# Kernel tuning notes

Measured on AMD Instinct MI355X. Metric: run time of the kernel, lower is better.

The kernel has to match this reference:

```python
import jax, jax.numpy as jnp
import numpy as np

B, T, I, H, O = 64, 512, 512, 512, 512

def setup_inputs() -> dict:
    key = jax.random.key(0)
    ks = jax.random.split(key, 8)
    s = lambda k, shape, fan: jax.random.normal(k, shape, dtype=jnp.float32) / np.sqrt(fan)
    return {
        "embeddings": jax.random.normal(ks[0], (B, T, I), dtype=jnp.float32),
        "last_logits": jax.random.normal(ks[1], (B, O), dtype=jnp.float32),
        "W_in": s(ks[2], (H, I), I),
        "b_in": jnp.zeros((H,), jnp.float32),
        "W_y": s(ks[3], (H, O), O),
        "b_y": jnp.zeros((H,), jnp.float32),
        "W_out": s(ks[4], (O, H), H),
        "b_out": jnp.zeros((O,), jnp.float32),
    }

def reference(embeddings, last_logits, W_in, b_in, W_y, b_y, W_out, b_out):
    # Precompute input projection for all timesteps: [B,T,H] -> scan axis [T,B,H]
    xin = jnp.einsum("bti,hi->bth", embeddings, W_in) + b_in
    xin = jnp.swapaxes(xin, 0, 1)  # [T,B,H]

    def step(y_t, xin_t):
        # Jordan cell: h_t = tanh(W_in x_t + W_y y_{t-1} + biases); y_t = W_out h_t + b_out
        h_t = jnp.tanh(xin_t + y_t @ W_y.T + b_y)
        y_new = h_t @ W_out.T + b_out
        return y_new, (h_t, y_new)

    y_last, (h_seq, y_seq) = jax.lax.scan(step, last_logits, xin)
    h = jnp.swapaxes(h_seq, 0, 1)  # [B,T,H]
    y = jnp.swapaxes(y_seq, 0, 1)  # [B,T,O]
    return h, y, y_last
```

## Files before the change

### kernel.cpp

```cpp
#include <hip/hip_runtime.h>
#include <hip/hip_bf16.h>
#include <stdint.h>

typedef unsigned short u16;
typedef unsigned int u32;
typedef unsigned long long u64;
typedef __attribute__((ext_vector_type(8))) short short8;
typedef __attribute__((ext_vector_type(4))) float f32x4;
typedef __attribute__((ext_vector_type(2))) float f32x2;
typedef __attribute__((ext_vector_type(4))) unsigned short u16x4;

__device__ __forceinline__ float bf2f(u16 h) {
    union { u32 u; float f; } c; c.u = ((u32)h) << 16; return c.f;
}
__device__ __forceinline__ u16 f2bf(float f) {
    union { float f; u32 u; } c; c.f = f;
    u32 u = c.u;
    return (u16)((u + 0x7fffu + ((u >> 16) & 1u)) >> 16);
}

__device__ __forceinline__ float fast_tanh(float x) {
    float ax = __builtin_fabsf(x);
    float arg = ax * 2.8853900817779268f;
    float p;
    asm("v_exp_f32 %0, %1" : "=v"(p) : "v"(arg));
    float q = p + 1.f;
    float r;
    asm("v_rcp_f32 %0, %1" : "=v"(r) : "v"(q));
    float t = 1.f - 2.f * r;
    return __builtin_copysignf(t, x);
}

__global__ void k_init(u32* h_ex) {
    uint4 v;
    v.x = 0x00010000u; v.y = 0x00010000u; v.z = 0x00010000u; v.w = 0x00010000u;
    ((uint4*)h_ex)[blockIdx.x * 256 + threadIdx.x] = v;
}

__global__ void k_c(const float* __restrict__ Wy, const float* __restrict__ bout,
                    const float* __restrict__ bin, const float* __restrict__ by,
                    float* __restrict__ cvec, float* __restrict__ biasE) {
    int i = blockIdx.x * 64 + threadIdx.x;
    const float* wr = Wy + (size_t)i * 512;
    float s = 0.f;
    for (int k = 0; k < 512; ++k) s += wr[k] * bout[k];
    cvec[i] = s;
    biasE[i] = s + bin[i] + by[i];
}

__global__ __launch_bounds__(512) void k_z0(const float* __restrict__ ll,
                                            const float* __restrict__ Wy,
                                            const float* __restrict__ cvec,
                                            float* __restrict__ z0mc) {
    __shared__ float lls[512];
    int b = blockIdx.x, i = threadIdx.x;
    lls[i] = ll[b * 512 + i];
    __syncthreads();
    const float* wr = Wy + (size_t)i * 512;
    float s = 0.f;
    for (int k = 0; k < 512; ++k) s += wr[k] * lls[k];
    z0mc[(size_t)b * 512 + i] = s - cvec[i];
}

__global__ __launch_bounds__(256) void k_split(const float* __restrict__ in,
                                               u16* __restrict__ hi,
                                               u16* __restrict__ lo) {
    int i = blockIdx.x * 256 + threadIdx.x;
    float v = in[i];
    u16 h = f2bf(v);
    hi[i] = h;
    lo[i] = f2bf(v - bf2f(h));
}

__global__ __launch_bounds__(256) void k_tsplit(const float* __restrict__ in,
                                                u16* __restrict__ hi,
                                                u16* __restrict__ lo) {
    __shared__ float tile[32][33];
    int bx = blockIdx.x, by = blockIdx.y;
    int tx = threadIdx.x & 31, ty = threadIdx.x >> 5;
    for (int i = 0; i < 32; i += 8)
        tile[ty + i][tx] = in[(size_t)(by * 32 + ty + i) * 512 + bx * 32 + tx];
    __syncthreads();
    for (int i = 0; i < 32; i += 8) {
        float v = tile[tx][ty + i];
        size_t idx = (size_t)(bx * 32 + ty + i) * 512 + by * 32 + tx;
        u16 h = f2bf(v);
        hi[idx] = h;
        lo[idx] = f2bf(v - bf2f(h));
    }
}

__global__ __launch_bounds__(256) void gemm3(
    const void* __restrict__ Aptr, int a_fp32,
    const u16* __restrict__ Bhi, const u16* __restrict__ Blo,
    u16* __restrict__ out_hi, u16* __restrict__ out_lo,
    float* __restrict__ out_f,
    const float* __restrict__ bias, int mode) {
    __shared__ u16 AsHi[128 * 32];
    __shared__ u16 AsLo[128 * 32];
    __shared__ u16 BsHi[128 * 32];
    __shared__ u16 BsLo[128 * 32];
    const int tid = threadIdx.x;
    const int lane = tid & 63;
    const int w = tid >> 6;
    const int wm = w & 1, wn = w >> 1;
    const int quad = lane >> 4, l15 = lane & 15;
    const int tx = blockIdx.x, tn = blockIdx.y;

    f32x4 acc[4][4];
    f32x4 zero4 = {0.f, 0.f, 0.f, 0.f};
#pragma unroll
    for (int i = 0; i < 4; ++i)
#pragma unroll
        for (int j = 0; j < 4; ++j) acc[i][j] = zero4;

    const float* Af = (const float*)Aptr;
    const u16* Ab = (const u16*)Aptr;
    const int s0 = tid, s1 = tid + 256;

    for (int kk = 0; kk < 16; ++kk) {
        const uint4* BgH = (const uint4*)(Bhi + (size_t)tn * 128 * 512 + kk * 32);
        const uint4* BgL = (const uint4*)(Blo + (size_t)tn * 128 * 512 + kk * 32);
        uint4 bh0 = BgH[(s0 >> 2) * 64 + (s0 & 3)];
        uint4 bh1 = BgH[(s1 >> 2) * 64 + (s1 & 3)];
        uint4 bl0 = BgL[(s0 >> 2) * 64 + (s0 & 3)];
        uint4 bl1 = BgL[(s1 >> 2) * 64 + (s1 & 3)];
        f32x4 av[4];
        uint4 ab0, ab1;
        if (a_fp32) {
            const float* Agf = Af + (size_t)tx * 128 * 512 + kk * 32;
#pragma unroll
            for (int p = 0; p < 4; ++p) {
                int f = tid + p * 256;
                av[p] = *(const f32x4*)(Agf + (f >> 3) * 512 + (f & 7) * 4);
            }
        } else {
            const uint4* Ag = (const uint4*)(Ab + (size_t)tx * 128 * 512 + kk * 32);
            ab0 = Ag[(s0 >> 2) * 64 + (s0 & 3)];
            ab1 = Ag[(s1 >> 2) * 64 + (s1 & 3)];
        }
        __syncthreads();
        ((uint4*)BsHi)[s0] = bh0; ((uint4*)BsHi)[s1] = bh1;
        ((uint4*)BsLo)[s0] = bl0; ((uint4*)BsLo)[s1] = bl1;
        if (a_fp32) {
#pragma unroll
            for (int p = 0; p < 4; ++p) {
                int f = tid + p * 256;
                u16x4 hi4, lo4;
#pragma unroll
                for (int j = 0; j < 4; ++j) {
                    float v = av[p][j];
                    u16 hh = f2bf(v);
                    hi4[j] = hh;
                    lo4[j] = f2bf(v - bf2f(hh));
                }
                int off = (f >> 3) * 32 + (f & 7) * 4;
                *(u16x4*)(AsHi + off) = hi4;
                *(u16x4*)(AsLo + off) = lo4;
            }
        } else {
            ((uint4*)AsHi)[s0] = ab0;
            ((uint4*)AsHi)[s1] = ab1;
        }
        __syncthreads();

        short8 afh[4], afl[4], bfh[4], bfl[4];
#pragma unroll
        for (int mi = 0; mi < 4; ++mi) {
            afh[mi] = *(const short8*)(AsHi + (wm * 64 + mi * 16 + l15) * 32 + quad * 8);
            if (a_fp32)
                afl[mi] = *(const short8*)(AsLo + (wm * 64 + mi * 16 + l15) * 32 + quad * 8);
        }
#pragma unroll
        for (int ni = 0; ni < 4; ++ni) {
            bfh[ni] = *(const short8*)(BsHi + (wn * 64 + ni * 16 + l15) * 32 + quad * 8);
            bfl[ni] = *(const short8*)(BsLo + (wn * 64 + ni * 16 + l15) * 32 + quad * 8);
        }
#pragma unroll
        for (int mi = 0; mi < 4; ++mi)
#pragma unroll
            for (int ni = 0; ni < 4; ++ni) {
                acc[mi][ni] = __builtin_amdgcn_mfma_f32_16x16x32_bf16(
                    afh[mi], bfh[ni], acc[mi][ni], 0, 0, 0);
                acc[mi][ni] = __builtin_amdgcn_mfma_f32_16x16x32_bf16(
                    afh[mi], bfl[ni], acc[mi][ni], 0, 0, 0);
                if (a_fp32)
                    acc[mi][ni] = __builtin_amdgcn_mfma_f32_16x16x32_bf16(
                        afl[mi], bfh[ni], acc[mi][ni], 0, 0, 0);
            }
    }

#pragma unroll
    for (int mi = 0; mi < 4; ++mi) {
#pragma unroll
        for (int ni = 0; ni < 4; ++ni) {
            int col = tn * 128 + wn * 64 + ni * 16 + l15;
            float bv = (mode == 1) ? bias[col] : 0.f;
#pragma unroll
            for (int r = 0; r < 4; ++r) {
                int row = tx * 128 + wm * 64 + mi * 16 + quad * 4 + r;
                float v = acc[mi][ni][r] + bv;
                size_t idx = (size_t)row * 512 + col;
                if (mode == 0) {
                    u16 hi = f2bf(v);
                    out_hi[idx] = hi;
                    out_lo[idx] = f2bf(v - bf2f(hi));
                } else {
                    out_f[idx] = v;
                }
            }
        }
    }
}

__global__ __launch_bounds__(256, 1) void k_scan(
    const u16* __restrict__ Mhi, const u16* __restrict__ Mlo,
    float* e_io,
    const float* __restrict__ z0mc,
    u32* h_ex)
{
    __shared__ float zpart[2 * 4 * 4 * 64];

    const int tid = threadIdx.x;
    const int lane = tid & 63, w = tid >> 6;
    const int quad = lane >> 4, l15 = lane & 15;
    const int g = blockIdx.x & 3, s = blockIdx.x >> 2;

    short8 mf[2][4][2];
#pragma unroll
    for (int nt = 0; nt < 2; ++nt)
#pragma unroll
        for (int kap = 0; kap < 4; ++kap) {
            size_t off = ((size_t)(s * 32 + nt * 16 + l15)) * 512 +
                         (w * 128 + kap * 32 + quad * 8);
            mf[nt][kap][0] = *(const short8*)(Mhi + off);
            mf[nt][kap][1] = *(const short8*)(Mlo + off);
        }

    const int erow = tid >> 4;
    const int ec0 = (tid & 15) * 2;
    const int bb = g * 16 + erow;

    f32x2 ecur = *(const f32x2*)(e_io + ((size_t)bb * 512 + 0) * 512 + s * 32 + ec0);

#pragma unroll 1
    for (int t = 0; t < 512; ++t) {
        if (t > 0) {
            const u64* ex = (const u64*)(h_ex +
                (size_t)(((t - 1) & 1) * 4 + g) * 8192);
            const u64* p0 = ex + (size_t)(l15 * 512 + w * 128 + quad * 8) / 2;
            const u64 tagmask = (1ull << 16) | (1ull << 48);
            const u64 tagval = (((t - 1) >> 1) & 1) ? tagmask : 0ull;
            {
                const u64* pc = p0 + (size_t)quad * 16;
                for (;;) {
                    u64 c = __hip_atomic_load(pc, __ATOMIC_RELAXED,
                                              __HIP_MEMORY_SCOPE_AGENT);
                    if (__all(((c ^ tagval) & tagmask) == 0)) break;
                }
            }
            u64 d[4][4];
            for (;;) {
#pragma unroll
                for (int kap = 0; kap < 4; ++kap) {
                    const u64* p = p0 + kap * 16;
#pragma unroll
                    for (int j = 0; j < 4; ++j)
                        d[kap][j] = __hip_atomic_load(p + j, __ATOMIC_RELAXED,
                                                      __HIP_MEMORY_SCOPE_AGENT);
                }
                u64 bad = 0;
#pragma unroll
                for (int kap = 0; kap < 4; ++kap)
#pragma unroll
                    for (int j = 0; j < 4; ++j)
                        bad |= (d[kap][j] ^ tagval) & tagmask;
                if (__all(bad == 0)) break;
            }
            f32x4 accA[2], accB[2];
            f32x4 zero4 = {0.f, 0.f, 0.f, 0.f};
            accA[0] = zero4; accA[1] = zero4;
            accB[0] = zero4; accB[1] = zero4;
#pragma unroll
            for (int kap = 0; kap < 4; ++kap) {
                u32 qs[8] = {(u32)d[kap][0], (u32)(d[kap][0] >> 32),
                             (u32)d[kap][1], (u32)(d[kap][1] >> 32),
                             (u32)d[kap][2], (u32)(d[kap][2] >> 32),
                             (u32)d[kap][3], (u32)(d[kap][3] >> 32)};
                short8 ahi, alo;
#pragma unroll
                for (int j = 0; j < 8; ++j) {
                    ahi[j] = (short)(qs[j] & 0xffffu);
                    alo[j] = (short)(qs[j] >> 16);
                }
#pragma unroll
                for (int nt = 0; nt < 2; ++nt) {
                    f32x4* a = (kap < 2) ? &accA[nt] : &accB[nt];
                    *a = __builtin_amdgcn_mfma_f32_16x16x32_bf16(
                        ahi, mf[nt][kap][0], *a, 0, 0, 0);
                    *a = __builtin_amdgcn_mfma_f32_16x16x32_bf16(
                        alo, mf[nt][kap][0], *a, 0, 0, 0);
                    *a = __builtin_amdgcn_mfma_f32_16x16x32_bf16(
                        ahi, mf[nt][kap][1], *a, 0, 0, 0);
                }
            }
#pragma unroll
            for (int nt = 0; nt < 2; ++nt)
#pragma unroll
                for (int r = 0; r < 4; ++r)
                    zpart[((nt * 4 + w) * 4 + r) * 64 + lane] =
                        accA[nt][r] + accB[nt][r];
        }
        __syncthreads();

        {
            float hv[2];
#pragma unroll
            for (int cc = 0; cc < 2; ++cc) {
                int col = ec0 + cc;
                float z;
                if (t == 0) {
                    z = z0mc[(size_t)bb * 512 + s * 32 + col];
                } else {
                    int nt = col >> 4;
                    int lp = (erow >> 2) * 16 + (col & 15);
                    int rg = erow & 3;
                    z = zpart[((nt * 4 + 0) * 4 + rg) * 64 + lp] +
                        zpart[((nt * 4 + 1) * 4 + rg) * 64 + lp] +
                        zpart[((nt * 4 + 2) * 4 + rg) * 64 + lp] +
                        zpart[((nt * 4 + 3) * 4 + rg) * 64 + lp];
                }
                hv[cc] = fast_tanh(z + ecur[cc]);
            }
            u32 tag = (u32)((t >> 1) & 1);
            u32 pk[2];
#pragma unroll
            for (int cc = 0; cc < 2; ++cc) {
                u16 hi = f2bf(hv[cc]);
                u16 lo = f2bf(hv[cc] - bf2f(hi));
                lo = (u16)((lo & 0xFFFEu) | tag);
                pk[cc] = (((u32)lo) << 16) | (u32)hi;
            }
            u64 val = ((u64)pk[1] << 32) | pk[0];
            u64* dst = (u64*)(h_ex + (size_t)((t & 1) * 4 + g) * 8192 +
                              erow * 512 + s * 32 + ec0);
            __hip_atomic_store(dst, val, __ATOMIC_RELAXED,
                               __HIP_MEMORY_SCOPE_AGENT);
            size_t idx = ((size_t)bb * 512 + t) * 512 + s * 32 + ec0;
            f32x2 hw; hw[0] = hv[0]; hw[1] = hv[1];
            *(f32x2*)(e_io + idx) = hw;
            if (t < 511)
                ecur = *(const f32x2*)(e_io + idx + 512);
        }
        __asm__ volatile("" ::: "memory");
        __builtin_amdgcn_s_barrier();
        __asm__ volatile("" ::: "memory");
    }
}

__global__ __launch_bounds__(512) void k_ylast(const float* __restrict__ yreg,
                                               float* __restrict__ ylast) {
    int b = blockIdx.x, o = threadIdx.x;
    ylast[(size_t)b * 512 + o] = yreg[((size_t)b * 512 + 511) * 512 + o];
}

extern "C" void kernel_launch(void* const* d_in, const int* in_sizes, int n_in,
                              void* d_out, int out_size, void* d_ws, size_t ws_size,
                              hipStream_t stream) {
    const float* emb  = (const float*)d_in[0];
    const float* ll   = (const float*)d_in[1];
    const float* Win  = (const float*)d_in[2];
    const float* bin  = (const float*)d_in[3];
    const float* Wy   = (const float*)d_in[4];
    const float* by   = (const float*)d_in[5];
    const float* Wout = (const float*)d_in[6];
    const float* bout = (const float*)d_in[7];

    float* out = (float*)d_out;
    float* h_reg = out;
    float* y_reg = out + (size_t)16777216;
    float* ylast_reg = out + (size_t)33554432;

    char* ws = (char*)d_ws;
    size_t off = 0;
    u16* buf1 = (u16*)(ws + off); off += (size_t)512 * 512 * 2;
    u16* buf2 = (u16*)(ws + off); off += (size_t)512 * 512 * 2;
    u16* Mhi  = (u16*)(ws + off); off += (size_t)512 * 512 * 2;
    u16* Mlo  = (u16*)(ws + off); off += (size_t)512 * 512 * 2;
    float* z0mc  = (float*)(ws + off); off += (size_t)64 * 512 * 4;
    float* cvec  = (float*)(ws + off); off += 512 * 4;
    float* biasE = (float*)(ws + off); off += 512 * 4;
    u32* h_ex = (u32*)(ws + off); off += (size_t)2 * 4 * 8192 * 4;

    k_init<<<64, 256, 0, stream>>>(h_ex);
    k_c<<<8, 64, 0, stream>>>(Wy, bout, bin, by, cvec, biasE);
    k_z0<<<64, 512, 0, stream>>>(ll, Wy, cvec, z0mc);
    k_tsplit<<<dim3(16, 16), 256, 0, stream>>>(Wout, buf1, buf2);
    gemm3<<<dim3(4, 4), 256, 0, stream>>>(Wy, 1, buf1, buf2, Mhi, Mlo,
                                          nullptr, nullptr, 0);
    k_split<<<1024, 256, 0, stream>>>(Win, buf1, buf2);
    gemm3<<<dim3(256, 4), 256, 0, stream>>>(emb, 1, buf1, buf2, nullptr, nullptr,
                                            h_reg, biasE, 1);
    k_scan<<<64, 256, 0, stream>>>(Mhi, Mlo, h_reg, z0mc, h_ex);
    k_split<<<1024, 256, 0, stream>>>(Wout, buf1, buf2);
    gemm3<<<dim3(256, 4), 256, 0, stream>>>(h_reg, 1, buf1, buf2, nullptr, nullptr,
                                            y_reg, bout, 1);
    k_ylast<<<64, 512, 0, stream>>>(y_reg, ylast_reg);
}
```

Baseline: 2.113 ms.

## Split each block's batch into two half-groups and pipeline exchange with compute

The scan kernel now handles two 8-row batch groups per block instead of one 16-row group. It issues the cross-block exchange loads for one group while the MFMA and tanh work for the other group runs, so the global-memory wait overlaps with compute. It also uses perm instructions to unpack the hi/lo bf16 halves and drops the separate single-word spin before the full load. The cost is two barriers per timestep instead of one, and MFMA tiles that are half-used (only quads 0-1 write results), which roughly doubles MFMA issue per useful row.

```diff
diff --git a/kernel.cpp b/kernel.cpp
--- a/kernel.cpp
+++ b/kernel.cpp
@@ -219,12 +219,13 @@
     const float* __restrict__ z0mc,
     u32* h_ex)
 {
-    __shared__ float zpart[2 * 4 * 4 * 64];
+    __shared__ float zbuf[2][1024];
 
     const int tid = threadIdx.x;
     const int lane = tid & 63, w = tid >> 6;
     const int quad = lane >> 4, l15 = lane & 15;
-    const int g = blockIdx.x & 3, s = blockIdx.x >> 2;
+    const int q = blockIdx.x & 3, s = blockIdx.x >> 2;
+    const int gA = q, gB = q + 4;
 
     short8 mf[2][4][2];
 #pragma unroll
@@ -237,124 +238,146 @@
             mf[nt][kap][1] = *(const short8*)(Mlo + off);
         }
 
-    const int erow = tid >> 4;
-    const int ec0 = (tid & 15) * 2;
-    const int bb = g * 16 + erow;
-
-    f32x2 ecur = *(const f32x2*)(e_io + ((size_t)bb * 512 + 0) * 512 + s * 32 + ec0);
+    const int er = tid >> 5;
+    const int c = tid & 31;
+    const int gcol = s * 32 + c;
+    const int bbA = gA * 8 + er, bbB = gB * 8 + er;
+    const int pub_off = er * 512 + gcol;
+    const size_t lidx = (size_t)((l15 & 7) * 256 + w * 64 + quad * 4);
+
+    size_t eiA = (size_t)bbA * 512 * 512 + gcol;
+    size_t eiB = (size_t)bbB * 512 * 512 + gcol;
+    float ecA = e_io[eiA];
+    float ecB = e_io[eiB];
+
+    const u64 tagmask = (1ull << 16) | (1ull << 48);
+    u64 dA[4][4], dB[4][4];
+
+    auto issue16 = [&](u64 (&d)[4][4], const u64* p0) {
+#pragma unroll
+        for (int kap = 0; kap < 4; ++kap)
+#pragma unroll
+            for (int j = 0; j < 4; ++j)
+                d[kap][j] = __hip_atomic_load(p0 + kap * 16 + j, __ATOMIC_RELAXED,
+                                              __HIP_MEMORY_SCOPE_AGENT);
+    };
+    auto verify16 = [&](u64 (&d)[4][4], const u64* p0, u64 tagval) {
+        for (;;) {
+            u64 bad = 0;
+#pragma unroll
+            for (int kap = 0; kap < 4; ++kap)
+#pragma unroll
+                for (int j = 0; j < 4; ++j)
+                    bad |= (d[kap][j] ^ tagval) & tagmask;
+            if (__all(bad == 0)) break;
+            issue16(d, p0);
+        }
+    };
+    auto mfma_z = [&](const u64 (&d)[4][4], float* zp) {
+        f32x4 accA[2], accB[2];
+        f32x4 zero4 = {0.f, 0.f, 0.f, 0.f};
+        accA[0] = zero4; accA[1] = zero4;
+        accB[0] = zero4; accB[1] = zero4;
+#pragma unroll
+        for (int kap = 0; kap < 4; ++kap) {
+            u32 x0 = (u32)d[kap][0], x1 = (u32)(d[kap][0] >> 32);
+            u32 x2 = (u32)d[kap][1], x3 = (u32)(d[kap][1] >> 32);
+            u32 x4 = (u32)d[kap][2], x5 = (u32)(d[kap][2] >> 32);
+            u32 x6 = (u32)d[kap][3], x7 = (u32)(d[kap][3] >> 32);
+            union { short8 s8; u32 u[4]; } hi_, lo_;
+#if __has_builtin(__builtin_amdgcn_perm)
+            hi_.u[0] = __builtin_amdgcn_perm(x1, x0, 0x05040100u);
+            hi_.u[1] = __builtin_amdgcn_perm(x3, x2, 0x05040100u);
+            hi_.u[2] = __builtin_amdgcn_perm(x5, x4, 0x05040100u);
+            hi_.u[3] = __builtin_amdgcn_perm(x7, x6, 0x05040100u);
+            lo_.u[0] = __builtin_amdgcn_perm(x1, x0, 0x07060302u);
+            lo_.u[1] = __builtin_amdgcn_perm(x3, x2, 0x07060302u);
+            lo_.u[2] = __builtin_amdgcn_perm(x5, x4, 0x07060302u);
+            lo_.u[3] = __builtin_amdgcn_perm(x7, x6, 0x07060302u);
+#else
+            hi_.u[0] = ((x1 & 0xffffu) << 16) | (x0 & 0xffffu);
+            hi_.u[1] = ((x3 & 0xffffu) << 16) | (x2 & 0xffffu);
+            hi_.u[2] = ((x5 & 0xffffu) << 16) | (x4 & 0xffffu);
+            hi_.u[3] = ((x7 & 0xffffu) << 16) | (x6 & 0xffffu);
+            lo_.u[0] = (x1 & 0xffff0000u) | (x0 >> 16);
+            lo_.u[1] = (x3 & 0xffff0000u) | (x2 >> 16);
+            lo_.u[2] = (x5 & 0xffff0000u) | (x4 >> 16);
+            lo_.u[3] = (x7 & 0xffff0000u) | (x6 >> 16);
+#endif
+#pragma unroll
+            for (int nt = 0; nt < 2; ++nt) {
+                f32x4* a = (kap < 2) ? &accA[nt] : &accB[nt];
+                *a = __builtin_amdgcn_mfma_f32_16x16x32_bf16(
+                    hi_.s8, mf[nt][kap][0], *a, 0, 0, 0);
+                *a = __builtin_amdgcn_mfma_f32_16x16x32_bf16(
+                    lo_.s8, mf[nt][kap][0], *a, 0, 0, 0);
+                *a = __builtin_amdgcn_mfma_f32_16x16x32_bf16(
+                    hi_.s8, mf[nt][kap][1], *a, 0, 0, 0);
+            }
+        }
+        if (quad < 2) {
+#pragma unroll
+            for (int nt = 0; nt < 2; ++nt)
+#pragma unroll
+                for (int r = 0; r < 4; ++r)
+                    zp[((nt * 4 + w) * 4 + r) * 32 + quad * 16 + l15] =
+                        accA[nt][r] + accB[nt][r];
+        }
+    };
+    auto phase_bar = [&]() {
+        __asm__ volatile("s_waitcnt lgkmcnt(0)" ::: "memory");
+        __builtin_amdgcn_s_barrier();
+        __asm__ volatile("" ::: "memory");
+    };
+    auto finishP = [&](int t, int g, int bb, const float* zp, float& ecur,
+                       size_t& eidx) {
+        float z;
+        if (t == 0) {
+            z = z0mc[(size_t)bb * 512 + gcol];
+        } else {
+            int nt = c >> 4, rg = er & 3, q2 = er >> 2, cl = c & 15;
+            z = zp[((nt * 4 + 0) * 4 + rg) * 32 + q2 * 16 + cl] +
+                zp[((nt * 4 + 1) * 4 + rg) * 32 + q2 * 16 + cl] +
+                zp[((nt * 4 + 2) * 4 + rg) * 32 + q2 * 16 + cl] +
+                zp[((nt * 4 + 3) * 4 + rg) * 32 + q2 * 16 + cl];
+        }
+        float hval = fast_tanh(z + ecur);
+        u32 tag = (u32)((t >> 1) & 1);
+        u16 hi = f2bf(hval);
+        u16 lo = f2bf(hval - bf2f(hi));
+        lo = (u16)((lo & 0xFFFEu) | tag);
+        u32 pk = (((u32)lo) << 16) | (u32)hi;
+        __hip_atomic_store(h_ex + (size_t)((t & 1) * 8 + g) * 4096 + pub_off,
+                           pk, __ATOMIC_RELAXED, __HIP_MEMORY_SCOPE_AGENT);
+        e_io[eidx] = hval;
+        if (t < 511) ecur = e_io[eidx + 512];
+        eidx += 512;
+    };
 
 #pragma unroll 1
     for (int t = 0; t < 512; ++t) {
+        const int pprev = (t - 1) & 1, pcur = t & 1;
+        const u64 tv_prev = (((t - 1) >> 1) & 1) ? tagmask : 0ull;
         if (t > 0) {
-            const u64* ex = (const u64*)(h_ex +
-                (size_t)(((t - 1) & 1) * 4 + g) * 8192);
-            const u64* p0 = ex + (size_t)(l15 * 512 + w * 128 + quad * 8) / 2;
-            const u64 tagmask = (1ull << 16) | (1ull << 48);
-            const u64 tagval = (((t - 1) >> 1) & 1) ? tagmask : 0ull;
-            {
-                const u64* pc = p0 + (size_t)quad * 16;
-                for (;;) {
-                    u64 c = __hip_atomic_load(pc, __ATOMIC_RELAXED,
-                                              __HIP_MEMORY_SCOPE_AGENT);
-                    if (__all(((c ^ tagval) & tagmask) == 0)) break;
-                }
-            }
-            u64 d[4][4];
-            for (;;) {
-#pragma unroll
-                for (int kap = 0; kap < 4; ++kap) {
-                    const u64* p = p0 + kap * 16;
-#pragma unroll
-                    for (int j = 0; j < 4; ++j)
-                        d[kap][j] = __hip_atomic_load(p + j, __ATOMIC_RELAXED,
-                                                      __HIP_MEMORY_SCOPE_AGENT);
-                }
-                u64 bad = 0;
-#pragma unroll
-                for (int kap = 0; kap < 4; ++kap)
-#pragma unroll
-                    for (int j = 0; j < 4; ++j)
-                        bad |= (d[kap][j] ^ tagval) & tagmask;
-                if (__all(bad == 0)) break;
-            }
-            f32x4 accA[2], accB[2];
-            f32x4 zero4 = {0.f, 0.f, 0.f, 0.f};
-            accA[0] = zero4; accA[1] = zero4;
-            accB[0] = zero4; accB[1] = zero4;
-#pragma unroll
-            for (int kap = 0; kap < 4; ++kap) {
-                u32 qs[8] = {(u32)d[kap][0], (u32)(d[kap][0] >> 32),
-                             (u32)d[kap][1], (u32)(d[kap][1] >> 32),
-                             (u32)d[kap][2], (u32)(d[kap][2] >> 32),
-                             (u32)d[kap][3], (u32)(d[kap][3] >> 32)};
-                short8 ahi, alo;
-#pragma unroll
-                for (int j = 0; j < 8; ++j) {
-                    ahi[j] = (short)(qs[j] & 0xffffu);
-                    alo[j] = (short)(qs[j] >> 16);
-                }
-#pragma unroll
-                for (int nt = 0; nt < 2; ++nt) {
-                    f32x4* a = (kap < 2) ? &accA[nt] : &accB[nt];
-                    *a = __builtin_amdgcn_mfma_f32_16x16x32_bf16(
-                        ahi, mf[nt][kap][0], *a, 0, 0, 0);
-                    *a = __builtin_amdgcn_mfma_f32_16x16x32_bf16(
-                        alo, mf[nt][kap][0], *a, 0, 0, 0);
-                    *a = __builtin_amdgcn_mfma_f32_16x16x32_bf16(
-                        ahi, mf[nt][kap][1], *a, 0, 0, 0);
-                }
-            }
-#pragma unroll
-            for (int nt = 0; nt < 2; ++nt)
-#pragma unroll
-                for (int r = 0; r < 4; ++r)
-                    zpart[((nt * 4 + w) * 4 + r) * 64 + lane] =
-                        accA[nt][r] + accB[nt][r];
-        }
-        __syncthreads();
-
-        {
-            float hv[2];
-#pragma unroll
-            for (int cc = 0; cc < 2; ++cc) {
-                int col = ec0 + cc;
-                float z;
-                if (t == 0) {
-                    z = z0mc[(size_t)bb * 512 + s * 32 + col];
-                } else {
-                    int nt = col >> 4;
-                    int lp = (erow >> 2) * 16 + (col & 15);
-                    int rg = erow & 3;
-                    z = zpart[((nt * 4 + 0) * 4 + rg) * 64 + lp] +
-                        zpart[((nt * 4 + 1) * 4 + rg) * 64 + lp] +
-                        zpart[((nt * 4 + 2) * 4 + rg) * 64 + lp] +
-                        zpart[((nt * 4 + 3) * 4 + rg) * 64 + lp];
-                }
-                hv[cc] = fast_tanh(z + ecur[cc]);
-            }
-            u32 tag = (u32)((t >> 1) & 1);
-            u32 pk[2];
-#pragma unroll
-            for (int cc = 0; cc < 2; ++cc) {
-                u16 hi = f2bf(hv[cc]);
-                u16 lo = f2bf(hv[cc] - bf2f(hi));
-                lo = (u16)((lo & 0xFFFEu) | tag);
-                pk[cc] = (((u32)lo) << 16) | (u32)hi;
-            }
-            u64 val = ((u64)pk[1] << 32) | pk[0];
-            u64* dst = (u64*)(h_ex + (size_t)((t & 1) * 4 + g) * 8192 +
-                              erow * 512 + s * 32 + ec0);
-            __hip_atomic_store(dst, val, __ATOMIC_RELAXED,
-                               __HIP_MEMORY_SCOPE_AGENT);
-            size_t idx = ((size_t)bb * 512 + t) * 512 + s * 32 + ec0;
-            f32x2 hw; hw[0] = hv[0]; hw[1] = hv[1];
-            *(f32x2*)(e_io + idx) = hw;
-            if (t < 511)
-                ecur = *(const f32x2*)(e_io + idx + 512);
-        }
-        __asm__ volatile("" ::: "memory");
-        __builtin_amdgcn_s_barrier();
-        __asm__ volatile("" ::: "memory");
+            const u64* pA = (const u64*)h_ex + (size_t)(pprev * 8 + gA) * 2048 + lidx;
+            verify16(dA, pA, tv_prev);
+            mfma_z(dA, &zbuf[0][0]);
+            const u64* pB = (const u64*)h_ex + (size_t)(pprev * 8 + gB) * 2048 + lidx;
+            issue16(dB, pB);
+        }
+        phase_bar();
+        finishP(t, gA, bbA, &zbuf[0][0], ecA, eiA);
+        if (t > 0) {
+            const u64* pB = (const u64*)h_ex + (size_t)(pprev * 8 + gB) * 2048 + lidx;
+            verify16(dB, pB, tv_prev);
+            mfma_z(dB, &zbuf[1][0]);
+        }
+        if (t < 511) {
+            const u64* pAn = (const u64*)h_ex + (size_t)(pcur * 8 + gA) * 2048 + lidx;
+            issue16(dA, pAn);
+        }
+        phase_bar();
+        finishP(t, gB, bbB, &zbuf[1][0], ecB, eiB);
     }
 }
 
@@ -390,7 +413,7 @@
     float* z0mc  = (float*)(ws + off); off += (size_t)64 * 512 * 4;
     float* cvec  = (float*)(ws + off); off += 512 * 4;
     float* biasE = (float*)(ws + off); off += 512 * 4;
-    u32* h_ex = (u32*)(ws + off); off += (size_t)2 * 4 * 8192 * 4;
+    u32* h_ex = (u32*)(ws + off); off += (size_t)2 * 8 * 4096 * 4;
 
     k_init<<<64, 256, 0, stream>>>(h_ex);
     k_c<<<8, 64, 0, stream>>>(Wy, bout, bin, by, cvec, biasE);
```

After: 3.003 ms. +42.1%, slower.
